# Performance work log

Hardware: AMD Instinct MI355X
Metric: run time of the kernel (lower is better)

Reference implementation:

```python
import jax, jax.numpy as jnp
import numpy as np

B = 4
HIDDEN = 256
NH, NL, NP = 8, 4, 4
DH = HIDDEN // NH
IMG = 256
SHAPES = ((64, 64), (32, 32), (16, 16), (8, 8))
CHS = (128, 256, 512, 512)
T = 3
NLAYERS = 6
S = sum(h * w for h, w in SHAPES)


def conv2d(x, w, b, pad):
    y = jax.lax.conv_general_dilated(x, w, (1, 1), [(pad, pad), (pad, pad)],
                                     dimension_numbers=('NCHW', 'OIHW', 'NCHW'))
    return y + b[None, :, None, None]


def group_norm(x, g, beta, groups=32, eps=1e-5):
    b, c, h, w = x.shape
    xg = x.reshape(b, groups, c // groups, h, w)
    mu = xg.mean((2, 3, 4), keepdims=True)
    var = ((xg - mu) ** 2).mean((2, 3, 4), keepdims=True)
    xg = (xg - mu) * jax.lax.rsqrt(var + eps)
    return xg.reshape(b, c, h, w) * g[None, :, None, None] + beta[None, :, None, None]


def layer_norm(x, g, b, eps=1e-5):
    mu = x.mean(-1, keepdims=True)
    var = ((x - mu) ** 2).mean(-1, keepdims=True)
    return (x - mu) * jax.lax.rsqrt(var + eps) * g + b


def pos_embed_sine(h, w, num_feats=128, temp=10000.0):
    # PositionEmbeddingSine with normalize=True, mask all-False
    scale = 2.0 * np.pi
    eps = 1e-6
    y = jnp.arange(1, h + 1, dtype=jnp.float32) / (h + eps) * scale
    x = jnp.arange(1, w + 1, dtype=jnp.float32) / (w + eps) * scale
    yy = jnp.broadcast_to(y[:, None], (h, w))
    xx = jnp.broadcast_to(x[None, :], (h, w))
    dim_t = temp ** (2.0 * (jnp.arange(num_feats) // 2).astype(jnp.float32) / num_feats)
    px = xx[..., None] / dim_t
    py = yy[..., None] / dim_t
    px = jnp.stack([jnp.sin(px[..., 0::2]), jnp.cos(px[..., 1::2])], -1).reshape(h, w, num_feats)
    py = jnp.stack([jnp.sin(py[..., 0::2]), jnp.cos(py[..., 1::2])], -1).reshape(h, w, num_feats)
    return jnp.concatenate([py, px], -1)  # (h, w, 2*num_feats)


def ms_deform(value, locs, attw):
    # value: (B,S,NH,DH); locs: (B,S,NH,NL,NP,2) normalized xy; attw: (B,S,NH,NL,NP)
    out = jnp.zeros((B, S, NH, DH), value.dtype)
    start = 0
    for l, (h, w) in enumerate(SHAPES):
        v = value[:, start:start + h * w]  # (B,hw,NH,DH)
        start += h * w
        gx = locs[:, :, :, l, :, 0] * w - 0.5  # grid_sample align_corners=False
        gy = locs[:, :, :, l, :, 1] * h - 0.5  # (B,S,NH,NP)
        x0 = jnp.floor(gx)
        y0 = jnp.floor(gy)
        wx1 = gx - x0
        wy1 = gy - y0
        acc = jnp.zeros((B, S, NH, NP, DH), value.dtype)
        for dy in (0, 1):
            for dx in (0, 1):
                xi = x0 + dx
                yi = y0 + dy
                wgt = (wx1 if dx else 1.0 - wx1) * (wy1 if dy else 1.0 - wy1)
                valid = ((xi >= 0) & (xi < w) & (yi >= 0) & (yi < h)).astype(value.dtype)
                xi_c = jnp.clip(xi, 0, w - 1).astype(jnp.int32)
                yi_c = jnp.clip(yi, 0, h - 1).astype(jnp.int32)
                idx = yi_c * w + xi_c  # (B,S,NH,NP)
                idx2 = idx.transpose(0, 1, 3, 2).reshape(B, S * NP, NH, 1)
                samp = jnp.take_along_axis(v, idx2, axis=1)  # (B,S*NP,NH,DH)
                samp = samp.reshape(B, S, NP, NH, DH).transpose(0, 1, 3, 2, 4)
                acc = acc + samp * (wgt * valid)[..., None]
        out = out + (acc * attw[:, :, :, l, :, None]).sum(3)
    return out.reshape(B, S, NH * DH)


def _forward(feat_t0_l0, feat_t0_l1, feat_t0_l2, feat_t0_l3,
             feat_t1_l0, feat_t1_l1, feat_t1_l2, feat_t1_l3,
             feat_t2_l0, feat_t2_l1, feat_t2_l2, feat_t2_l3,
             tfw,
             proj_w0, proj_b0, gn_g0, gn_b0,
             proj_w1, proj_b1, gn_g1, gn_b1,
             proj_w2, proj_b2, gn_g2, gn_b2,
             proj_w3, proj_b3, gn_g3, gn_b3,
             level_embed,
             off_w, off_b, aw_w, aw_b, val_w, val_b, out_w, out_b,
             ln1_g, ln1_b, ff1_w, ff1_b, ff2_w, ff2_b, ln2_g, ln2_b,
             c1_w, c1_b, c2_w, c2_b):
    feats = [[feat_t0_l0, feat_t0_l1, feat_t0_l2, feat_t0_l3],
             [feat_t1_l0, feat_t1_l1, feat_t1_l2, feat_t1_l3],
             [feat_t2_l0, feat_t2_l1, feat_t2_l2, feat_t2_l3]]
    proj = [(proj_w0, proj_b0, gn_g0, gn_b0), (proj_w1, proj_b1, gn_g1, gn_b1),
            (proj_w2, proj_b2, gn_g2, gn_b2), (proj_w3, proj_b3, gn_g3, gn_b3)]
    priors = (0, CHS[0], CHS[1], CHS[2])  # replicates original (buggy) prior indexing
    srcs, poss = [], []
    for l in range(NL):
        atf = jnp.stack([feats[t][l] for t in range(T)], 1)  # (B,T,C,H,W)
        wsl = jax.nn.softmax(tfw[:, priors[l]:priors[l] + CHS[l]], axis=0)  # (T,C)
        fused = (atf * wsl[None, :, :, None, None]).sum(1)
        pw, pb, gg, gb = proj[l]
        x = group_norm(conv2d(fused, pw, pb, 0), gg, gb)  # 1x1 proj + GN
        h, w = SHAPES[l]
        srcs.append(x.reshape(B, HIDDEN, h * w).transpose(0, 2, 1))
        pe = pos_embed_sine(h, w).reshape(h * w, HIDDEN) + level_embed[l]
        poss.append(jnp.broadcast_to(pe[None], (B, h * w, HIDDEN)))
    src = jnp.concatenate(srcs, 1)  # (B,S,256)
    pos = jnp.concatenate(poss, 1)
    # reference points (valid_ratios == 1 since masks are all False)
    refs = []
    for (h, w) in SHAPES:
        gy, gx = jnp.meshgrid((jnp.arange(h) + 0.5) / h, (jnp.arange(w) + 0.5) / w, indexing='ij')
        refs.append(jnp.stack([gx.ravel(), gy.ravel()], -1))
    ref = jnp.broadcast_to(jnp.concatenate(refs, 0)[None, :, None, :], (B, S, NL, 2)).astype(jnp.float32)
    norm_wh = jnp.array([[w, h] for (h, w) in SHAPES], jnp.float32)  # (NL,2) xy
    for i in range(NLAYERS):
        q = src + pos
        off = (q @ off_w[i].T + off_b[i]).reshape(B, S, NH, NL, NP, 2)
        aw = jax.nn.softmax((q @ aw_w[i].T + aw_b[i]).reshape(B, S, NH, NL * NP), -1).reshape(B, S, NH, NL, NP)
        val = (src @ val_w[i].T + val_b[i]).reshape(B, S, NH, DH)
        locs = ref[:, :, None, :, None, :] + off / norm_wh[None, None, None, :, None, :]
        attn = ms_deform(val, locs, aw) @ out_w[i].T + out_b[i]
        src = layer_norm(src + attn, ln1_g[i], ln1_b[i])
        ff = (jax.nn.relu(src @ ff1_w[i].T + ff1_b[i])) @ ff2_w[i].T + ff2_b[i]
        src = layer_norm(src + ff, ln2_g[i], ln2_b[i])
    h0, w0 = SHAPES[0]
    layer0 = src[:, :h0 * w0, :].reshape(B, h0, w0, HIDDEN).transpose(0, 3, 1, 2)
    pred = conv2d(jax.nn.relu(conv2d(layer0, c1_w, c1_b, 1)), c2_w, c2_b, 1)
    return jax.image.resize(pred, (B, pred.shape[1], IMG, IMG), method='bilinear')


def setup_inputs():
    key = jax.random.key(0)
    ks = iter(jax.random.split(key, 128))
    d = {}
    for t in range(T):
        for l, ((h, w), c) in enumerate(zip(SHAPES, CHS)):
            d['feat_t%d_l%d' % (t, l)] = jax.random.normal(next(ks), (B, c, h, w), jnp.float32)
    d['tfw'] = jax.random.normal(next(ks), (T, sum(CHS)), jnp.float32)
    for l, c in enumerate(CHS):
        d['proj_w%d' % l] = jax.random.normal(next(ks), (HIDDEN, c, 1, 1), jnp.float32) * 0.02
        d['proj_b%d' % l] = jnp.zeros((HIDDEN,), jnp.float32)
        d['gn_g%d' % l] = jnp.ones((HIDDEN,), jnp.float32)
        d['gn_b%d' % l] = jnp.zeros((HIDDEN,), jnp.float32)
    d['level_embed'] = jax.random.normal(next(ks), (NL, HIDDEN), jnp.float32)
    Lc = NLAYERS

    def w(shape, s=0.02):
        return jax.random.normal(next(ks), shape, jnp.float32) * s
    d['off_w'] = w((Lc, NH * NL * NP * 2, HIDDEN))
    d['off_b'] = w((Lc, NH * NL * NP * 2), 0.1)
    d['aw_w'] = w((Lc, NH * NL * NP, HIDDEN))
    d['aw_b'] = w((Lc, NH * NL * NP), 0.1)
    d['val_w'] = w((Lc, HIDDEN, HIDDEN))
    d['val_b'] = jnp.zeros((Lc, HIDDEN), jnp.float32)
    d['out_w'] = w((Lc, HIDDEN, HIDDEN))
    d['out_b'] = jnp.zeros((Lc, HIDDEN), jnp.float32)
    d['ln1_g'] = jnp.ones((Lc, HIDDEN), jnp.float32)
    d['ln1_b'] = jnp.zeros((Lc, HIDDEN), jnp.float32)
    d['ff1_w'] = w((Lc, 1024, HIDDEN))
    d['ff1_b'] = jnp.zeros((Lc, 1024), jnp.float32)
    d['ff2_w'] = w((Lc, HIDDEN, 1024))
    d['ff2_b'] = jnp.zeros((Lc, HIDDEN), jnp.float32)
    d['ln2_g'] = jnp.ones((Lc, HIDDEN), jnp.float32)
    d['ln2_b'] = jnp.zeros((Lc, HIDDEN), jnp.float32)
    d['c1_w'] = w((64, HIDDEN, 3, 3))
    d['c1_b'] = jnp.zeros((64,), jnp.float32)
    d['c2_w'] = w((2, 64, 3, 3))
    d['c2_b'] = jnp.zeros((2,), jnp.float32)
    return d


def reference(feat_t0_l0, feat_t0_l1, feat_t0_l2, feat_t0_l3,
              feat_t1_l0, feat_t1_l1, feat_t1_l2, feat_t1_l3,
              feat_t2_l0, feat_t2_l1, feat_t2_l2, feat_t2_l3,
              tfw,
              proj_w0, proj_b0, gn_g0, gn_b0,
              proj_w1, proj_b1, gn_g1, gn_b1,
              proj_w2, proj_b2, gn_g2, gn_b2,
              proj_w3, proj_b3, gn_g3, gn_b3,
              level_embed,
              off_w, off_b, aw_w, aw_b, val_w, val_b, out_w, out_b,
              ln1_g, ln1_b, ff1_w, ff1_b, ff2_w, ff2_b, ln2_g, ln2_b,
              c1_w, c1_b, c2_w, c2_b):
    return _forward(feat_t0_l0, feat_t0_l1, feat_t0_l2, feat_t0_l3,
                    feat_t1_l0, feat_t1_l1, feat_t1_l2, feat_t1_l3,
                    feat_t2_l0, feat_t2_l1, feat_t2_l2, feat_t2_l3,
                    tfw,
                    proj_w0, proj_b0, gn_g0, gn_b0,
                    proj_w1, proj_b1, gn_g1, gn_b1,
                    proj_w2, proj_b2, gn_g2, gn_b2,
                    proj_w3, proj_b3, gn_g3, gn_b3,
                    level_embed,
                    off_w, off_b, aw_w, aw_b, val_w, val_b, out_w, out_b,
                    ln1_g, ln1_b, ff1_w, ff1_b, ff2_w, ff2_b, ln2_g, ln2_b,
                    c1_w, c1_b, c2_w, c2_b)
```

## Files before the change

### kernel.cpp

```cpp
#include <hip/hip_runtime.h>
#include <math.h>

constexpr int kB = 4;
constexpr int kS = 5440;
constexpr int kH = 256;
constexpr int kNH = 8, kNL = 4, kNP = 4, kDH = 32;
constexpr int kM = kB * kS;
constexpr int kCHSUM = 1408;

typedef __attribute__((ext_vector_type(8))) short short8v;
typedef __attribute__((ext_vector_type(4))) short short4v;
typedef __attribute__((ext_vector_type(4))) float f32x4;
typedef __attribute__((ext_vector_type(2))) float fx2;
typedef __attribute__((ext_vector_type(16))) float f32x16;

__device__ inline short bf16rne(float f) {
    unsigned u = __float_as_uint(f);
    u += 0x7FFF + ((u >> 16) & 1);
    return (short)(u >> 16);
}
__device__ inline float bf2f(short s) {
    return __uint_as_float(((unsigned)(unsigned short)s) << 16);
}
__device__ inline int xcd_swz(int orig, int nwg) {
    int q = nwg >> 3, r = nwg & 7;
    int x = orig & 7, o = orig >> 3;
    return (x < r ? x*(q+1) : r*(q+1) + (x-r)*q) + o;
}
#define LSWZ(row, chunk) ((row)*40 + ((chunk) ^ ((row) & 24)))

__device__ inline void cv4(const float* __restrict__ in, short* __restrict__ out, int q)
{
    int i = q * 4;
    f32x4 v = *(const f32x4*)(in + i);
    short4v o;
    o[0]=bf16rne(v[0]); o[1]=bf16rne(v[1]); o[2]=bf16rne(v[2]); o[3]=bf16rne(v[3]);
    *(short4v*)(out + i) = o;
}
__global__ __launch_bounds__(256) void prep_all_kernel(
        const float* __restrict__ off_w, const float* __restrict__ aw_w,
        const float* __restrict__ off_b, const float* __restrict__ aw_b,
        const float* __restrict__ val_w, const float* __restrict__ out_w,
        const float* __restrict__ ff1w, const float* __restrict__ ff2w,
        const float* __restrict__ pw0, const float* __restrict__ pw1,
        const float* __restrict__ pw2, const float* __restrict__ pw3,
        const float* __restrict__ c1w, const float* __restrict__ c2w,
        short* __restrict__ Wcat, float* __restrict__ bcat,
        short* __restrict__ valwb, short* __restrict__ outwb,
        short* __restrict__ ff1wb, short* __restrict__ ff2wb,
        short* __restrict__ pwb, short* __restrict__ c1wb, float* __restrict__ c2wr)
{
    int idx = blockIdx.x * 256 + threadIdx.x;
    if (idx < 589824) {
        int col = idx & 255;
        int row = (idx >> 8) % 384;
        int i   = idx / (384*256);
        float v = (row < 256) ? off_w[((size_t)i*256 + row)*256 + col]
                              : aw_w[((size_t)i*128 + row-256)*256 + col];
        Wcat[idx] = bf16rne(v);
        return;
    }
    idx -= 589824;
    if (idx < 2304) {
        int row = idx % 384, i = idx / 384;
        bcat[idx] = (row < 256) ? off_b[i*256 + row] : aw_b[i*128 + row-256];
        return;
    }
    idx -= 2304;
    if (idx < 98304) { cv4(val_w, valwb, idx); return; }
    idx -= 98304;
    if (idx < 98304) { cv4(out_w, outwb, idx); return; }
    idx -= 98304;
    if (idx < 393216) { cv4(ff1w, ff1wb, idx); return; }
    idx -= 393216;
    if (idx < 393216) { cv4(ff2w, ff2wb, idx); return; }
    idx -= 393216;
    if (idx < 8192)  { cv4(pw0, pwb + 0,      idx); return; }
    idx -= 8192;
    if (idx < 16384) { cv4(pw1, pwb + 32768,  idx); return; }
    idx -= 16384;
    if (idx < 32768) { cv4(pw2, pwb + 98304,  idx); return; }
    idx -= 32768;
    if (idx < 32768) { cv4(pw3, pwb + 229376, idx); return; }
    idx -= 32768;
    if (idx < 147456) {
        int k = idx % 2304, o = idx / 2304;
        int kblk = k >> 8, c = k & 255;
        c1wb[idx] = bf16rne(c1w[(size_t)o*2304 + c*9 + kblk]);
        return;
    }
    idx -= 147456;
    if (idx < 1152) {
        int c = idx & 63, r = idx >> 6;
        int o = r / 9, kblk = r % 9;
        c2wr[idx] = c2w[((size_t)o*64 + c)*9 + kblk];
    }
}
constexpr int kPrepThreads = 589824+2304+98304+98304+393216+393216+8192+16384+32768+32768+147456+1152;


__global__ __launch_bounds__(256) void fuseT_kernel(const float* __restrict__ f0,
        const float* __restrict__ f1, const float* __restrict__ f2,
        const float* __restrict__ tfw, short* __restrict__ out,
        int c, int hw, int prior)
{
    __shared__ float tile[32][33];
    int p0 = blockIdx.x * 32;
    int c0 = blockIdx.y * 32;
    int b  = blockIdx.z;
    int tx  = threadIdx.x & 31;
    int ty8 = threadIdx.x >> 5;
    #pragma unroll
    for (int i = 0; i < 4; ++i) {
        int ch = c0 + ty8 + i*8;
        float t0 = tfw[0*kCHSUM + prior + ch];
        float t1 = tfw[1*kCHSUM + prior + ch];
        float t2 = tfw[2*kCHSUM + prior + ch];
        float m = fmaxf(t0, fmaxf(t1, t2));
        float e0 = expf(t0-m), e1 = expf(t1-m), e2 = expf(t2-m);
        float inv = 1.0f / (e0+e1+e2);
        size_t base = ((size_t)b*c + ch)*hw + p0 + tx;
        tile[ty8+i*8][tx] = f0[base]*(e0*inv) + f1[base]*(e1*inv) + f2[base]*(e2*inv);
    }
    __syncthreads();
    #pragma unroll
    for (int i = 0; i < 4; ++i) {
        int p = p0 + ty8 + i*8;
        out[((size_t)b*hw + p)*c + c0 + tx] = bf16rne(tile[tx][ty8+i*8]);
    }
}

__global__ __launch_bounds__(256) void gn_sum_kernel(const float* __restrict__ xbufT,
        float* __restrict__ gnstat, int nchunks)
{
    int chunk = blockIdx.x, b = blockIdx.y;
    int t = threadIdx.x;
    size_t base = ((size_t)b*nchunks + chunk) * 4096;
    float s = 0.f, q = 0.f;
    #pragma unroll
    for (int i = 0; i < 4; ++i) {
        f32x4 v = *(const f32x4*)(xbufT + base + i*1024 + t*4);
        s += v[0]+v[1]+v[2]+v[3];
        q += v[0]*v[0]+v[1]*v[1]+v[2]*v[2]+v[3]*v[3];
    }
    __shared__ float ls[256], lq[256];
    ls[t] = s; lq[t] = q; __syncthreads();
    if (t < 64) { ls[t] += ls[t+64]+ls[t+128]+ls[t+192];
                  lq[t] += lq[t+64]+lq[t+128]+lq[t+192]; }
    __syncthreads();
    if (t < 32) {
        float ss = ls[2*t] + ls[2*t+1];
        float qq = lq[2*t] + lq[2*t+1];
        size_t o = (((size_t)b*nchunks + chunk)*32 + t)*2;
        gnstat[o] = ss; gnstat[o+1] = qq;
    }
}

__global__ __launch_bounds__(256) void gn_fin_kernel(const float* __restrict__ gnstat,
        const float* __restrict__ gg, const float* __restrict__ gb,
        float* __restrict__ gnA, float* __restrict__ gnB, int nchunks, int hw)
{
    int b = blockIdx.x, t = threadIdx.x;
    int g = t >> 3, sub = t & 7;
    float s = 0.f, q = 0.f;
    for (int c = sub; c < nchunks; c += 8) {
        size_t o = (((size_t)b*nchunks + c)*32 + g)*2;
        s += gnstat[o]; q += gnstat[o+1];
    }
    __shared__ float ls[256], lq[256], gmu[32], ginv[32];
    ls[t] = s; lq[t] = q; __syncthreads();
    if (sub < 4) { ls[t] += ls[t+4]; lq[t] += lq[t+4]; } __syncthreads();
    if (sub < 2) { ls[t] += ls[t+2]; lq[t] += lq[t+2]; } __syncthreads();
    if (sub == 0) {
        float ss = ls[t] + ls[t+1], qq = lq[t] + lq[t+1];
        float n = 8.0f * hw;
        float mu = ss / n;
        float var = qq / n - mu*mu;
        gmu[g] = mu; ginv[g] = rsqrtf(var + 1e-5f);
    }
    __syncthreads();
    int ch = t;
    float A = ginv[ch>>3] * gg[ch];
    float B = gb[ch] - gmu[ch>>3] * A;
    gnA[b*256 + ch] = A;
    gnB[b*256 + ch] = B;
}

__global__ __launch_bounds__(256) void gn_apply_kernel(const float* __restrict__ xbufT,
        const float* __restrict__ gnA, const float* __restrict__ gnB,
        const float* __restrict__ pos, float* __restrict__ src,
        short* __restrict__ srcbf, short* __restrict__ qbf, int hw, int sbase)
{
    int E = hw * 256;
    size_t fl = (size_t)blockIdx.x*1024 + threadIdx.x*4;
    int b = (int)(fl / E);
    int off = (int)(fl - (size_t)b*E);
    int p = off >> 8, col = off & 255;
    f32x4 v = *(const f32x4*)(xbufT + fl);
    f32x4 A = *(const f32x4*)(gnA + b*256 + col);
    f32x4 Bv = *(const f32x4*)(gnB + b*256 + col);
    size_t si = ((size_t)b*kS + sbase + p)*256 + col;
    f32x4 pv = *(const f32x4*)(pos + si);
    f32x4 o;
    o[0]=v[0]*A[0]+Bv[0]; o[1]=v[1]*A[1]+Bv[1];
    o[2]=v[2]*A[2]+Bv[2]; o[3]=v[3]*A[3]+Bv[3];
    *(f32x4*)(src + si) = o;
    short4v sb, qb;
    sb[0]=bf16rne(o[0]); sb[1]=bf16rne(o[1]); sb[2]=bf16rne(o[2]); sb[3]=bf16rne(o[3]);
    qb[0]=bf16rne(o[0]+pv[0]); qb[1]=bf16rne(o[1]+pv[1]);
    qb[2]=bf16rne(o[2]+pv[2]); qb[3]=bf16rne(o[3]+pv[3]);
    *(short4v*)(srcbf + si) = sb;
    *(short4v*)(qbf + si) = qb;
}

__global__ __launch_bounds__(256) void pos_all_kernel(const float* __restrict__ lev,
                                                      float* __restrict__ pos)
{
    int idx = blockIdx.x * 256 + threadIdx.x;
    if (idx >= kS * 256) return;
    int ch = idx & 255;
    int p  = idx >> 8;
    int lvl, py, px, dim;
    if (p < 4096)      { lvl = 0; dim = 64; int l = p;        py = l >> 6; px = l & 63; }
    else if (p < 5120) { lvl = 1; dim = 32; int l = p - 4096; py = l >> 5; px = l & 31; }
    else if (p < 5376) { lvl = 2; dim = 16; int l = p - 5120; py = l >> 4; px = l & 15; }
    else               { lvl = 3; dim = 8;  int l = p - 5376; py = l >> 3; px = l & 7; }
    int c2 = ch & 127;
    int i  = c2 >> 1;
    float invdt = exp2f((float)i * -0.20762050593046015f);
    float t;
    if (ch < 128) t = (py + 1) / ((float)dim + 1e-6f) * 6.2831853071795864f;
    else          t = (px + 1) / ((float)dim + 1e-6f) * 6.2831853071795864f;
    float arg = t * invdt;
    float val = (c2 & 1) ? cosf(arg) : sinf(arg);
    val += lev[lvl*kH + ch];
    #pragma unroll
    for (int b = 0; b < kB; ++b)
        pos[(size_t)b*kS*256 + idx] = val;
}

template<int BM, int OUTMODE>
__global__ __launch_bounds__(256) void gemm32(const short* __restrict__ A,
        const short* __restrict__ W, const float* __restrict__ bias,
        float* __restrict__ C, short* __restrict__ Cb, int N, int K, int relu, int ncols)
{
    constexpr int FI = BM / 64;
    constexpr int NAV = (BM == 128) ? 4 : 2;
    __shared__ short Asm[2][BM * 40];
    __shared__ short Bsm[2][128 * 40];
    const int lin = xcd_swz(blockIdx.x, gridDim.x);
    const int bn  = (lin % ncols) * 128;
    const int bm  = (lin / ncols) * BM;
    const int t    = threadIdx.x;
    const int lane = t & 63;
    const int wid  = t >> 6;
    const int wr   = wid >> 1;
    const int wc   = wid & 1;
    const int l31  = lane & 31;
    const int hi8  = (lane >> 5) * 8;

    f32x16 acc[FI][2];
    #pragma unroll
    for (int i = 0; i < FI; ++i)
        #pragma unroll
        for (int j = 0; j < 2; ++j)
            acc[i][j] = (f32x16){0,0,0,0,0,0,0,0,0,0,0,0,0,0,0,0};

    int sa_r, sa_k;
    if constexpr (BM == 128) { sa_r = t >> 1; sa_k = (t & 1) * 32; }
    else                     { sa_r = t >> 2; sa_k = (t & 3) * 16; }
    const short* Aptr = A + (size_t)(bm + sa_r)*K + sa_k;
    const int sb_r = t >> 1;
    const int sb_k = (t & 1) * 32;
    const short* Wptr = W + (size_t)(bn + sb_r)*K + sb_k;

    short8v a[NAV], b[4];
    #pragma unroll
    for (int v = 0; v < NAV; ++v) a[v] = *(const short8v*)(Aptr + v*8);
    #pragma unroll
    for (int v = 0; v < 4; ++v)   b[v] = *(const short8v*)(Wptr + v*8);

    for (int k0 = 0; k0 < K; k0 += 64) {
        __syncthreads();
        if constexpr (BM == 128) {
            #pragma unroll
            for (int v = 0; v < 4; ++v) *(short8v*)&Asm[t & 1][LSWZ(sa_r, v*8)] = a[v];
        } else {
            #pragma unroll
            for (int v = 0; v < 2; ++v)
                *(short8v*)&Asm[sa_k >> 5][LSWZ(sa_r, (sa_k & 16) + v*8)] = a[v];
        }
        #pragma unroll
        for (int v = 0; v < 4; ++v) *(short8v*)&Bsm[t & 1][LSWZ(sb_r, v*8)] = b[v];
        __syncthreads();
        if (k0 + 64 < K) {
            #pragma unroll
            for (int v = 0; v < NAV; ++v) a[v] = *(const short8v*)(Aptr + k0 + 64 + v*8);
            #pragma unroll
            for (int v = 0; v < 4; ++v)   b[v] = *(const short8v*)(Wptr + k0 + 64 + v*8);
        }
        #pragma unroll
        for (int p = 0; p < 2; ++p)
            #pragma unroll
            for (int ks = 0; ks < 2; ++ks) {
                short8v af[FI], bfv[2];
                #pragma unroll
                for (int i = 0; i < FI; ++i)
                    af[i] = *(const short8v*)&Asm[p][LSWZ(wr*(BM/2) + i*32 + l31, ks*16 + hi8)];
                #pragma unroll
                for (int j = 0; j < 2; ++j)
                    bfv[j] = *(const short8v*)&Bsm[p][LSWZ(wc*64 + j*32 + l31, ks*16 + hi8)];
                #pragma unroll
                for (int i = 0; i < FI; ++i)
                    #pragma unroll
                    for (int j = 0; j < 2; ++j)
                        acc[i][j] = __builtin_amdgcn_mfma_f32_32x32x16_bf16(af[i], bfv[j], acc[i][j], 0, 0, 0);
            }
    }

    const int rbase = 4 * (lane >> 5);
    #pragma unroll
    for (int j = 0; j < 2; ++j) {
        int col = bn + wc*64 + j*32 + l31;
        float bz = bias[col];
        #pragma unroll
        for (int i = 0; i < FI; ++i) {
            int row0 = bm + wr*(BM/2) + i*32 + rbase;
            #pragma unroll
            for (int r = 0; r < 16; ++r) {
                int row = row0 + (r & 3) + 8*(r >> 2);
                float v = acc[i][j][r] + bz;
                if (relu) v = fmaxf(v, 0.f);
                if constexpr (OUTMODE == 0) C[(size_t)row*N + col] = v;
                else                        Cb[(size_t)row*N + col] = bf16rne(v);
            }
        }
    }
}

__global__ __launch_bounds__(256) void gemm_qv32(const short* __restrict__ Aq,
        const short* __restrict__ As, const short* __restrict__ W1,
        const short* __restrict__ W2, const float* __restrict__ b1,
        const float* __restrict__ b2, float* __restrict__ C1,
        short* __restrict__ Cb2)
{
    __shared__ short Asm[2][128 * 40];
    __shared__ short Bsm[2][128 * 40];
    const int lin = xcd_swz(blockIdx.x, gridDim.x);
    const int bn  = (lin % 5) * 128;
    const int bm  = (lin / 5) * 128;
    const bool qreg = bn < 384;
    const int K = 256;
    const int t    = threadIdx.x;
    const int lane = t & 63;
    const int wid  = t >> 6;
    const int wr   = wid >> 1;
    const int wc   = wid & 1;
    const int l31  = lane & 31;
    const int hi8  = (lane >> 5) * 8;
    const int sa_r = t >> 1;
    const int sa_p = t & 1;

    f32x16 acc[2][2];
    #pragma unroll
    for (int i = 0; i < 2; ++i)
        #pragma unroll
        for (int j = 0; j < 2; ++j)
            acc[i][j] = (f32x16){0,0,0,0,0,0,0,0,0,0,0,0,0,0,0,0};

    const short* Aptr = (qreg ? Aq : As) + (size_t)(bm + sa_r)*K + sa_p*32;
    const short* Wptr = (qreg ? (W1 + (size_t)(bn + sa_r)*K)
                              : (W2 + (size_t)(bn - 384 + sa_r)*K)) + sa_p*32;
    short8v a[4], b[4];
    #pragma unroll
    for (int v = 0; v < 4; ++v) { a[v] = *(const short8v*)(Aptr + v*8);
                                  b[v] = *(const short8v*)(Wptr + v*8); }

    for (int k0 = 0; k0 < K; k0 += 64) {
        __syncthreads();
        #pragma unroll
        for (int v = 0; v < 4; ++v) {
            *(short8v*)&Asm[sa_p][LSWZ(sa_r, v*8)] = a[v];
            *(short8v*)&Bsm[sa_p][LSWZ(sa_r, v*8)] = b[v];
        }
        __syncthreads();
        if (k0 + 64 < K) {
            #pragma unroll
            for (int v = 0; v < 4; ++v) {
                a[v] = *(const short8v*)(Aptr + k0 + 64 + v*8);
                b[v] = *(const short8v*)(Wptr + k0 + 64 + v*8);
            }
        }
        #pragma unroll
        for (int p = 0; p < 2; ++p)
            #pragma unroll
            for (int ks = 0; ks < 2; ++ks) {
                short8v af[2], bfv[2];
                #pragma unroll
                for (int i = 0; i < 2; ++i)
                    af[i] = *(const short8v*)&Asm[p][LSWZ(wr*64 + i*32 + l31, ks*16 + hi8)];
                #pragma unroll
                for (int j = 0; j < 2; ++j)
                    bfv[j] = *(const short8v*)&Bsm[p][LSWZ(wc*64 + j*32 + l31, ks*16 + hi8)];
                #pragma unroll
                for (int i = 0; i < 2; ++i)
                    #pragma unroll
                    for (int j = 0; j < 2; ++j)
                        acc[i][j] = __builtin_amdgcn_mfma_f32_32x32x16_bf16(af[i], bfv[j], acc[i][j], 0, 0, 0);
            }
    }

    const int rbase = 4 * (lane >> 5);
    if (bn == 256) {
        #pragma unroll
        for (int j = 0; j < 2; ++j) {
            int col = bn + wc*64 + j*32 + l31;
            float bz = b1[col];
            #pragma unroll
            for (int i = 0; i < 2; ++i) {
                int row0 = bm + wr*64 + i*32 + rbase;
                #pragma unroll
                for (int r = 0; r < 16; ++r) {
                    int row = row0 + (r & 3) + 8*(r >> 2);
                    float v = acc[i][j][r] + bz;
                    float m = v;
                    m = fmaxf(m, __shfl_xor(m, 1));
                    m = fmaxf(m, __shfl_xor(m, 2));
                    m = fmaxf(m, __shfl_xor(m, 4));
                    m = fmaxf(m, __shfl_xor(m, 8));
                    float e = expf(v - m);
                    float s = e;
                    s += __shfl_xor(s, 1);
                    s += __shfl_xor(s, 2);
                    s += __shfl_xor(s, 4);
                    s += __shfl_xor(s, 8);
                    C1[(size_t)row*384 + col] = e / s;
                }
            }
        }
    } else {
        #pragma unroll
        for (int j = 0; j < 2; ++j) {
            int col = bn + wc*64 + j*32 + l31;
            float bz = qreg ? b1[col] : b2[col - 384];
            #pragma unroll
            for (int i = 0; i < 2; ++i) {
                int row0 = bm + wr*64 + i*32 + rbase;
                #pragma unroll
                for (int r = 0; r < 16; ++r) {
                    int row = row0 + (r & 3) + 8*(r >> 2);
                    float v = acc[i][j][r] + bz;
                    if (qreg) C1[(size_t)row*384 + col] = v;
                    else      Cb2[(size_t)row*256 + col - 384] = bf16rne(v);
                }
            }
        }
    }
}

__global__ __launch_bounds__(256) void conv1_gemm_kernel(const short* __restrict__ srcbf,
        const short* __restrict__ Wr, const float* __restrict__ bias,
        float* __restrict__ C)
{
    __shared__ short Asm[2][128 * 40];
    __shared__ short Bsm[2][64 * 40];
    const int t    = threadIdx.x;
    const int bm   = blockIdx.x * 128;
    const int K    = 2304;
    const int lane = t & 63;
    const int wid  = t >> 6;
    const int wr   = wid >> 1;
    const int wc   = wid & 1;
    const int frow = lane & 15;
    const int g    = lane >> 4;
    const int sa_r = t >> 1;
    const int sa_p = t & 1;

    const int m  = bm + sa_r;
    const int bb = m >> 12, ys = (m >> 6) & 63, xs = m & 63;

    f32x4 acc[4][2];
    #pragma unroll
    for (int i = 0; i < 4; ++i)
        #pragma unroll
        for (int j = 0; j < 2; ++j)
            acc[i][j] = (f32x4){0.f,0.f,0.f,0.f};

    auto loadA = [&](int k0, short8v* r) {
        int kk = k0 + sa_p*32;
        int kblk = kk >> 8;
        int dyy = kblk / 3, dxx = kblk - dyy*3;
        int yy = ys + dyy - 1, xx = xs + dxx - 1;
        if (yy >= 0 && yy < 64 && xx >= 0 && xx < 64) {
            const short* p = srcbf + ((size_t)(bb*kS + yy*64 + xx))*256 + (kk & 255);
            #pragma unroll
            for (int v = 0; v < 4; ++v) r[v] = *(const short8v*)(p + v*8);
        } else {
            #pragma unroll
            for (int v = 0; v < 4; ++v) r[v] = (short8v){0,0,0,0,0,0,0,0};
        }
    };

    const int sb_r = t >> 2, sb_p = (t & 3) >> 1, sb_o = (t & 1) * 16;
    const short* Wptr = Wr + (size_t)sb_r*K + (t & 3)*16;
    short8v a[4], b[2];
    loadA(0, a);
    b[0] = *(const short8v*)Wptr;
    b[1] = *(const short8v*)(Wptr + 8);

    for (int k0 = 0; k0 < K; k0 += 64) {
        __syncthreads();
        #pragma unroll
        for (int v = 0; v < 4; ++v) *(short8v*)&Asm[sa_p][sa_r*40 + v*8] = a[v];
        *(short8v*)&Bsm[sb_p][sb_r*40 + sb_o]     = b[0];
        *(short8v*)&Bsm[sb_p][sb_r*40 + sb_o + 8] = b[1];
        __syncthreads();
        if (k0 + 64 < K) {
            loadA(k0 + 64, a);
            b[0] = *(const short8v*)(Wptr + k0 + 64);
            b[1] = *(const short8v*)(Wptr + k0 + 72);
        }
        #pragma unroll
        for (int p = 0; p < 2; ++p) {
            short8v af[4], bfv[2];
            #pragma unroll
            for (int i = 0; i < 4; ++i)
                af[i] = *(const short8v*)&Asm[p][(wr*64 + i*16 + frow)*40 + g*8];
            #pragma unroll
            for (int j = 0; j < 2; ++j)
                bfv[j] = *(const short8v*)&Bsm[p][(wc*32 + j*16 + frow)*40 + g*8];
            #pragma unroll
            for (int i = 0; i < 4; ++i)
                #pragma unroll
                for (int j = 0; j < 2; ++j)
                    acc[i][j] = __builtin_amdgcn_mfma_f32_16x16x32_bf16(af[i], bfv[j], acc[i][j], 0, 0, 0);
        }
    }

    #pragma unroll
    for (int j = 0; j < 2; ++j) {
        int col = wc*32 + j*16 + frow;
        float bz = bias[col];
        #pragma unroll
        for (int i = 0; i < 4; ++i) {
            int row = bm + wr*64 + i*16 + g*4;
            #pragma unroll
            for (int rr = 0; rr < 4; ++rr) {
                float v = fmaxf(acc[i][j][rr] + bz, 0.f);
                C[(size_t)(row + rr)*64 + col] = v;
            }
        }
    }
}

__global__ __launch_bounds__(256) void msdeform8_kernel(const short* __restrict__ val,
        const float* __restrict__ cat, short* __restrict__ msd)
{
    int blk  = xcd_swz(blockIdx.x, gridDim.x);
    int tid  = threadIdx.x;
    int d8   = tid & 3;
    int head = (tid >> 2) & 7;
    int bs   = blk*8 + (tid >> 5);
    int s  = bs % kS;
    int b  = bs / kS;
    float refx, refy;
    if (s < 4096)      { int loc = s;        refy = ((loc>>6)+0.5f)/64.f; refx = ((loc&63)+0.5f)/64.f; }
    else if (s < 5120) { int loc = s - 4096; refy = ((loc>>5)+0.5f)/32.f; refx = ((loc&31)+0.5f)/32.f; }
    else if (s < 5376) { int loc = s - 5120; refy = ((loc>>4)+0.5f)/16.f; refx = ((loc&15)+0.5f)/16.f; }
    else               { int loc = s - 5376; refy = ((loc>>3)+0.5f)/8.f;  refx = ((loc&7)+0.5f)/8.f; }
    const float* op = cat + (size_t)bs*384 + head*32;
    const float* ap = cat + (size_t)bs*384 + 256 + head*16;
    const short* vb = val + (size_t)b*kS*256 + head*32 + d8*8;
    const int WL[4] = {64,32,16,8};
    const int BASE[4] = {0,4096,5120,5376};
    fx2 acc0 = {0.f,0.f}, acc1 = {0.f,0.f}, acc2 = {0.f,0.f}, acc3 = {0.f,0.f};
    #pragma unroll
    for (int l = 0; l < 4; ++l) {
        int wl = WL[l], base = BASE[l];
        f32x4 o0 = *(const f32x4*)(op + l*8);
        f32x4 o1 = *(const f32x4*)(op + l*8 + 4);
        f32x4 av = *(const f32x4*)(ap + l*4);
        float oxs[4] = {o0[0], o0[2], o1[0], o1[2]};
        float oys[4] = {o0[1], o0[3], o1[1], o1[3]};
        #pragma unroll
        for (int p = 0; p < 4; ++p) {
            float gx = (refx + oxs[p]/wl)*wl - 0.5f;
            float gy = (refy + oys[p]/wl)*wl - 0.5f;
            float x0f = floorf(gx), y0f = floorf(gy);
            float wx1 = gx - x0f, wy1 = gy - y0f;
            int x0 = (int)x0f, y0 = (int)y0f;
            float a = av[p];
            #pragma unroll
            for (int dy = 0; dy < 2; ++dy) {
                int yi = y0 + dy;
                float wy = dy ? wy1 : 1.f - wy1;
                int vyok = (yi >= 0) & (yi < wl);
                int yc = min(max(yi, 0), wl - 1);
                #pragma unroll
                for (int dx = 0; dx < 2; ++dx) {
                    int xi = x0 + dx;
                    float wx = dx ? wx1 : 1.f - wx1;
                    int vok = vyok & (xi >= 0) & (xi < wl);
                    int xc = min(max(xi, 0), wl - 1);
                    float wgt = vok ? wx*wy*a : 0.f;
                    fx2 w2 = {wgt, wgt};
                    uint4 v = *(const uint4*)&vb[(size_t)(base + yc*wl + xc)*256];
                    fx2 t0, t1, t2, t3;
                    t0[0]=__uint_as_float(v.x << 16); t0[1]=__uint_as_float(v.x & 0xffff0000u);
                    t1[0]=__uint_as_float(v.y << 16); t1[1]=__uint_as_float(v.y & 0xffff0000u);
                    t2[0]=__uint_as_float(v.z << 16); t2[1]=__uint_as_float(v.z & 0xffff0000u);
                    t3[0]=__uint_as_float(v.w << 16); t3[1]=__uint_as_float(v.w & 0xffff0000u);
                    acc0 = t0 * w2 + acc0;
                    acc1 = t1 * w2 + acc1;
                    acc2 = t2 * w2 + acc2;
                    acc3 = t3 * w2 + acc3;
                }
            }
        }
    }
    short8v o;
    o[0]=bf16rne(acc0[0]); o[1]=bf16rne(acc0[1]);
    o[2]=bf16rne(acc1[0]); o[3]=bf16rne(acc1[1]);
    o[4]=bf16rne(acc2[0]); o[5]=bf16rne(acc2[1]);
    o[6]=bf16rne(acc3[0]); o[7]=bf16rne(acc3[1]);
    *(short8v*)&msd[(size_t)bs*256 + head*32 + d8*8] = o;
}

template<int WQ>
__global__ __launch_bounds__(256) void add_ln_kernel(float* __restrict__ src,
        const short* __restrict__ delta, const float* __restrict__ g,
        const float* __restrict__ bta, short* __restrict__ srcbf,
        short* __restrict__ qbf, const float* __restrict__ pos)
{
    int lane = threadIdx.x & 63;
    int row  = blockIdx.x*4 + (threadIdx.x >> 6);
    f32x4* s4 = (f32x4*)(src + (size_t)row*256);
    f32x4 x = s4[lane];
    short4v dd = *(const short4v*)&delta[(size_t)row*256 + lane*4];
    x[0]+=bf2f(dd[0]); x[1]+=bf2f(dd[1]); x[2]+=bf2f(dd[2]); x[3]+=bf2f(dd[3]);
    float s = x[0]+x[1]+x[2]+x[3];
    #pragma unroll
    for (int o = 1; o < 64; o <<= 1) s += __shfl_xor(s, o);
    float mu = s * (1.f/256.f);
    f32x4 xc;
    xc[0]=x[0]-mu; xc[1]=x[1]-mu; xc[2]=x[2]-mu; xc[3]=x[3]-mu;
    float s2 = xc[0]*xc[0]+xc[1]*xc[1]+xc[2]*xc[2]+xc[3]*xc[3];
    #pragma unroll
    for (int o = 1; o < 64; o <<= 1) s2 += __shfl_xor(s2, o);
    float inv = rsqrtf(s2*(1.f/256.f) + 1e-5f);
    const f32x4 gv = ((const f32x4*)g)[lane];
    const f32x4 bv = ((const f32x4*)bta)[lane];
    f32x4 o4;
    o4[0]=xc[0]*inv*gv[0]+bv[0]; o4[1]=xc[1]*inv*gv[1]+bv[1];
    o4[2]=xc[2]*inv*gv[2]+bv[2]; o4[3]=xc[3]*inv*gv[3]+bv[3];
    s4[lane] = o4;
    short4v sb;
    sb[0]=bf16rne(o4[0]); sb[1]=bf16rne(o4[1]); sb[2]=bf16rne(o4[2]); sb[3]=bf16rne(o4[3]);
    *(short4v*)&srcbf[(size_t)row*256 + lane*4] = sb;
    if constexpr (WQ) {
        f32x4 pv = ((const f32x4*)(pos + (size_t)row*256))[lane];
        short4v qb;
        qb[0]=bf16rne(o4[0]+pv[0]); qb[1]=bf16rne(o4[1]+pv[1]);
        qb[2]=bf16rne(o4[2]+pv[2]); qb[3]=bf16rne(o4[3]+pv[3]);
        *(short4v*)&qbf[(size_t)row*256 + lane*4] = qb;
    }
}

__global__ void conv2_kernel(const float* __restrict__ c1, const float* __restrict__ w,
                             const float* __restrict__ bias, float* __restrict__ pred)
{
    int idx = blockIdx.x * blockDim.x + threadIdx.x;
    int x = idx & 63;
    int y = (idx >> 6) & 63;
    int o = (idx >> 12) & 1;
    int b = idx >> 13;
    float acc = bias[o];
    #pragma unroll
    for (int dy = 0; dy < 3; ++dy) {
        int yy = y + dy - 1;
        if (yy < 0 || yy >= 64) continue;
        #pragma unroll
        for (int dx = 0; dx < 3; ++dx) {
            int xx = x + dx - 1;
            if (xx < 0 || xx >= 64) continue;
            const f32x4* sp = (const f32x4*)(c1 + ((size_t)(b*4096) + yy*64 + xx)*64);
            const f32x4* wp = (const f32x4*)(w + (o*9 + dy*3 + dx)*64);
            #pragma unroll
            for (int c = 0; c < 16; ++c) {
                f32x4 sv = sp[c], wv = wp[c];
                acc += sv[0]*wv[0] + sv[1]*wv[1] + sv[2]*wv[2] + sv[3]*wv[3];
            }
        }
    }
    pred[idx] = acc;
}

__global__ void resize_kernel(const float* __restrict__ pred, float* __restrict__ out)
{
    int idx = blockIdx.x * blockDim.x + threadIdx.x;
    int X = idx & 255;
    int Y = (idx >> 8) & 255;
    int c = (idx >> 16) & 1;
    int b = idx >> 17;
    float sx = (X + 0.5f)*0.25f - 0.5f;
    float sy = (Y + 0.5f)*0.25f - 0.5f;
    int x0 = (int)floorf(sx); float fx = sx - x0;
    int y0 = (int)floorf(sy); float fy = sy - y0;
    int x0c = min(max(x0, 0), 63), x1c = min(max(x0+1, 0), 63);
    int y0c = min(max(y0, 0), 63), y1c = min(max(y0+1, 0), 63);
    const float* p = pred + ((size_t)(b*2 + c))*4096;
    float v00 = p[y0c*64 + x0c], v01 = p[y0c*64 + x1c];
    float v10 = p[y1c*64 + x0c], v11 = p[y1c*64 + x1c];
    out[idx] = (1.f-fy)*((1.f-fx)*v00 + fx*v01) + fy*((1.f-fx)*v10 + fx*v11);
}

extern "C" void kernel_launch(void* const* d_in, const int* in_sizes, int n_in,
                              void* d_out, int out_size, void* d_ws, size_t ws_size,
                              hipStream_t stream)
{
    const float* F[3][4];
    for (int t = 0; t < 3; ++t)
        for (int l = 0; l < 4; ++l)
            F[t][l] = (const float*)d_in[t*4 + l];
    const float* tfw = (const float*)d_in[12];
    const float *pw[4], *pb[4], *gg[4], *gb[4];
    for (int l = 0; l < 4; ++l) {
        pw[l] = (const float*)d_in[13 + 4*l];
        pb[l] = (const float*)d_in[14 + 4*l];
        gg[l] = (const float*)d_in[15 + 4*l];
        gb[l] = (const float*)d_in[16 + 4*l];
    }
    const float* lev   = (const float*)d_in[29];
    const float* off_w = (const float*)d_in[30];
    const float* off_b = (const float*)d_in[31];
    const float* aw_w  = (const float*)d_in[32];
    const float* aw_b  = (const float*)d_in[33];
    const float* val_w = (const float*)d_in[34];
    const float* val_b = (const float*)d_in[35];
    const float* out_w = (const float*)d_in[36];
    const float* out_b = (const float*)d_in[37];
    const float* ln1g  = (const float*)d_in[38];
    const float* ln1b  = (const float*)d_in[39];
    const float* ff1w  = (const float*)d_in[40];
    const float* ff1b  = (const float*)d_in[41];
    const float* ff2w  = (const float*)d_in[42];
    const float* ff2b  = (const float*)d_in[43];
    const float* ln2g  = (const float*)d_in[44];
    const float* ln2b  = (const float*)d_in[45];
    const float* c1w   = (const float*)d_in[46];
    const float* c1b   = (const float*)d_in[47];
    const float* c2w   = (const float*)d_in[48];
    const float* c2b   = (const float*)d_in[49];

    const size_t N256 = (size_t)kB * kS * 256;
    float* ws    = (float*)d_ws;
    float* src   = ws;
    short* srcbf = (short*)(src + N256);
    short* qbf   = srcbf + N256;
    short* valbf = qbf + N256;
    short* msdbf = valbf + N256;
    short* warena= msdbf + N256;
    short* Wcat_bf = warena;
    short* valw_bf = Wcat_bf + 589824;
    short* outw_bf = valw_bf + 393216;
    short* ff1w_bf = outw_bf + 393216;
    short* ff2w_bf = ff1w_bf + 1572864;
    short* pw_bf   = ff2w_bf + 1572864;
    short* c1w_bf  = pw_bf + 360448;
    float* bcat  = (float*)(c1w_bf + 147456 + 128);
    float* gnstat= bcat + 4096;
    float* gnA   = gnstat + 65536;
    float* gnB   = gnA + 1024;
    float* c2wr  = gnB + 1024;
    float* pos   = c2wr + 1280;
    float* cat   = pos + N256;
    float* tmp   = cat + (size_t)kM*384;
    short* tmpbf = (short*)tmp;
    short* ffhbf = (short*)(tmp + N256);
    short* fusedT = (short*)cat;
    float* xbufT  = tmp;
    float* c1o   = (float*)valbf;
    float* pred  = (float*)msdbf;

    const int LVL_HWS[4]  = {4096, 1024, 256, 64};
    const int LVL_BASE[4] = {0, 4096, 5120, 5376};
    const int LVL_C[4]    = {128, 256, 512, 512};
    const int LVL_PRIOR[4]= {0, 128, 256, 512};
    const int PW_OFF[4]   = {0, 32768, 98304, 229376};

    prep_all_kernel<<<(kPrepThreads + 255)/256, 256, 0, stream>>>(
        off_w, aw_w, off_b, aw_b, val_w, out_w, ff1w, ff2w,
        pw[0], pw[1], pw[2], pw[3], c1w, c2w,
        Wcat_bf, bcat, valw_bf, outw_bf, ff1w_bf, ff2w_bf, pw_bf, c1w_bf, c2wr);

    pos_all_kernel<<<(kS*256 + 255)/256, 256, 0, stream>>>(lev, pos);
    for (int l = 0; l < 4; ++l) {
        int hw = LVL_HWS[l], c = LVL_C[l];
        dim3 gf(hw/32, c/32, kB);
        fuseT_kernel<<<gf, 256, 0, stream>>>(F[0][l], F[1][l], F[2][l], tfw,
                                             fusedT, c, hw, LVL_PRIOR[l]);
        int nwg = 2 * (kB*hw/64);
        gemm32<64,0><<<nwg, 256, 0, stream>>>(fusedT, pw_bf + PW_OFF[l], pb[l],
                                              xbufT, nullptr, 256, c, 0, 2);
        int nchunks = hw / 16;
        gn_sum_kernel<<<dim3(nchunks, kB), 256, 0, stream>>>(xbufT, gnstat, nchunks);
        gn_fin_kernel<<<kB, 256, 0, stream>>>(gnstat, gg[l], gb[l], gnA, gnB, nchunks, hw);
        gn_apply_kernel<<<(kB*hw*256)/1024, 256, 0, stream>>>(xbufT, gnA, gnB, pos,
                                                              src, srcbf, qbf, hw, LVL_BASE[l]);
    }

    for (int i = 0; i < 6; ++i) {
        gemm_qv32<<<5*(kM/128), 256, 0, stream>>>(qbf, srcbf,
                Wcat_bf + (size_t)i*384*256, valw_bf + (size_t)i*65536,
                bcat + i*384, val_b + i*256, cat, valbf);
        msdeform8_kernel<<<kM/8, 256, 0, stream>>>(valbf, cat, msdbf);
        gemm32<64,1><<<2*(kM/64), 256, 0, stream>>>(msdbf, outw_bf + (size_t)i*65536,
                                                    out_b + i*256, nullptr, tmpbf, 256, 256, 0, 2);
        add_ln_kernel<0><<<kM/4, 256, 0, stream>>>(src, tmpbf, ln1g + i*256, ln1b + i*256,
                                                   srcbf, nullptr, nullptr);
        gemm32<128,1><<<8*(kM/128), 256, 0, stream>>>(srcbf, ff1w_bf + (size_t)i*262144,
                                                      ff1b + i*1024, nullptr, ffhbf, 1024, 256, 1, 8);
        gemm32<64,1><<<2*(kM/64), 256, 0, stream>>>(ffhbf, ff2w_bf + (size_t)i*262144,
                                                    ff2b + i*256, nullptr, tmpbf, 256, 1024, 0, 2);
        add_ln_kernel<1><<<kM/4, 256, 0, stream>>>(src, tmpbf, ln2g + i*256, ln2b + i*256,
                                                   srcbf, qbf, pos);
    }

    {
        conv1_gemm_kernel<<<128, 256, 0, stream>>>(srcbf, c1w_bf, c1b, c1o);
        conv2_kernel<<<(kB*2*64*64)/256, 256, 0, stream>>>(c1o, c2wr, c2b, pred);
        resize_kernel<<<(kB*2*256*256)/256, 256, 0, stream>>>(pred, (float*)d_out);
    }
}
```

Before: 1.107 ms.

## Fuse output/FFN2 GEMMs with residual add and LayerNorm

Adds a gemm_ln kernel in which each block computes a full 64x256 output tile, adds bias and the residual, and does the LayerNorm reduction in registers and shared memory. It then writes src, srcbf and qbf directly, which removes the bf16 intermediate round trip and the separate add_ln launches. It also simplifies the sampling-coordinate math in msdeform and uses scalar fmas. In exchange, the grid has fewer blocks with wider N tiles, the accumulator is no longer rounded to bf16 before the residual add, and variance is computed as E[x^2]-mu^2.

Result: slower. 1.505 ms (+36.0%).

```diff
diff --git a/kernel.cpp b/kernel.cpp
--- a/kernel.cpp
+++ b/kernel.cpp
@@ -11,7 +11,6 @@
 typedef __attribute__((ext_vector_type(8))) short short8v;
 typedef __attribute__((ext_vector_type(4))) short short4v;
 typedef __attribute__((ext_vector_type(4))) float f32x4;
-typedef __attribute__((ext_vector_type(2))) float fx2;
 typedef __attribute__((ext_vector_type(16))) float f32x16;
 
 __device__ inline short bf16rne(float f) {
@@ -338,6 +337,129 @@
     }
 }
 
+template<int WQ>
+__global__ __launch_bounds__(256) void gemm_ln(const short* __restrict__ A,
+        const short* __restrict__ W, const float* __restrict__ bias,
+        const float* __restrict__ g, const float* __restrict__ bta,
+        float* __restrict__ src, short* __restrict__ srcbf,
+        short* __restrict__ qbf, const float* __restrict__ pos, int K)
+{
+    __shared__ short Asm[2][64 * 40];
+    __shared__ short Bsm[2][256 * 40];
+    __shared__ float lred[2][2][2][16][2];
+    const int t    = threadIdx.x;
+    const int bm   = blockIdx.x * 64;
+    const int lane = t & 63;
+    const int wid  = t >> 6;
+    const int wr   = wid >> 1;
+    const int wc   = wid & 1;
+    const int l31  = lane & 31;
+    const int hi   = lane >> 5;
+    const int hi8  = hi * 8;
+
+    f32x16 acc[4];
+    #pragma unroll
+    for (int j = 0; j < 4; ++j)
+        acc[j] = (f32x16){0,0,0,0,0,0,0,0,0,0,0,0,0,0,0,0};
+
+    const int sa_r = t >> 2;
+    const int sa_k = (t & 3) * 16;
+    const short* Aptr = A + (size_t)(bm + sa_r)*K + sa_k;
+    const short* Wptr = W + (size_t)t*K;
+
+    short8v a[2], b[8];
+    a[0] = *(const short8v*)(Aptr);
+    a[1] = *(const short8v*)(Aptr + 8);
+    #pragma unroll
+    for (int v = 0; v < 8; ++v) b[v] = *(const short8v*)(Wptr + v*8);
+
+    for (int k0 = 0; k0 < K; k0 += 64) {
+        __syncthreads();
+        *(short8v*)&Asm[sa_k >> 5][LSWZ(sa_r, (sa_k & 16) + 0)] = a[0];
+        *(short8v*)&Asm[sa_k >> 5][LSWZ(sa_r, (sa_k & 16) + 8)] = a[1];
+        #pragma unroll
+        for (int v = 0; v < 8; ++v)
+            *(short8v*)&Bsm[v >> 2][LSWZ(t, (v & 3)*8)] = b[v];
+        __syncthreads();
+        if (k0 + 64 < K) {
+            a[0] = *(const short8v*)(Aptr + k0 + 64);
+            a[1] = *(const short8v*)(Aptr + k0 + 72);
+            #pragma unroll
+            for (int v = 0; v < 8; ++v) b[v] = *(const short8v*)(Wptr + k0 + 64 + v*8);
+        }
+        #pragma unroll
+        for (int p = 0; p < 2; ++p)
+            #pragma unroll
+            for (int ks = 0; ks < 2; ++ks) {
+                short8v af = *(const short8v*)&Asm[p][LSWZ(wr*32 + l31, ks*16 + hi8)];
+                short8v bfv[4];
+                #pragma unroll
+                for (int j = 0; j < 4; ++j)
+                    bfv[j] = *(const short8v*)&Bsm[p][LSWZ(wc*128 + j*32 + l31, ks*16 + hi8)];
+                #pragma unroll
+                for (int j = 0; j < 4; ++j)
+                    acc[j] = __builtin_amdgcn_mfma_f32_32x32x16_bf16(af, bfv[j], acc[j], 0, 0, 0);
+            }
+    }
+
+    const int row0 = bm + wr*32 + 4*hi;
+    float rsum[16], rsq[16];
+    #pragma unroll
+    for (int r = 0; r < 16; ++r) { rsum[r] = 0.f; rsq[r] = 0.f; }
+    #pragma unroll
+    for (int j = 0; j < 4; ++j) {
+        int col = wc*128 + j*32 + l31;
+        float bz = bias[col];
+        #pragma unroll
+        for (int r = 0; r < 16; ++r) {
+            int row = row0 + (r & 3) + 8*(r >> 2);
+            float x = acc[j][r] + bz + src[(size_t)row*256 + col];
+            acc[j][r] = x;
+            rsum[r] += x;
+            rsq[r]  += x*x;
+        }
+    }
+    #pragma unroll
+    for (int o = 1; o < 32; o <<= 1) {
+        #pragma unroll
+        for (int r = 0; r < 16; ++r) {
+            rsum[r] += __shfl_xor(rsum[r], o);
+            rsq[r]  += __shfl_xor(rsq[r], o);
+        }
+    }
+    if (l31 == 0) {
+        #pragma unroll
+        for (int r = 0; r < 16; ++r) {
+            lred[wr][wc][hi][r][0] = rsum[r];
+            lred[wr][wc][hi][r][1] = rsq[r];
+        }
+    }
+    __syncthreads();
+    float mu[16], inv[16];
+    #pragma unroll
+    for (int r = 0; r < 16; ++r) {
+        float ts = rsum[r] + lred[wr][wc^1][hi][r][0];
+        float tq = rsq[r]  + lred[wr][wc^1][hi][r][1];
+        float m = ts * (1.f/256.f);
+        mu[r] = m;
+        inv[r] = rsqrtf(tq * (1.f/256.f) - m*m + 1e-5f);
+    }
+    #pragma unroll
+    for (int j = 0; j < 4; ++j) {
+        int col = wc*128 + j*32 + l31;
+        float gv = g[col], bv = bta[col];
+        #pragma unroll
+        for (int r = 0; r < 16; ++r) {
+            int row = row0 + (r & 3) + 8*(r >> 2);
+            size_t si = (size_t)row*256 + col;
+            float y = (acc[j][r] - mu[r]) * inv[r] * gv + bv;
+            src[si] = y;
+            srcbf[si] = bf16rne(y);
+            if constexpr (WQ) qbf[si] = bf16rne(y + pos[si]);
+        }
+    }
+}
+
 __global__ __launch_bounds__(256) void gemm_qv32(const short* __restrict__ Aq,
         const short* __restrict__ As, const short* __restrict__ W1,
         const short* __restrict__ W2, const float* __restrict__ b1,
@@ -573,10 +695,12 @@
     const short* vb = val + (size_t)b*kS*256 + head*32 + d8*8;
     const int WL[4] = {64,32,16,8};
     const int BASE[4] = {0,4096,5120,5376};
-    fx2 acc0 = {0.f,0.f}, acc1 = {0.f,0.f}, acc2 = {0.f,0.f}, acc3 = {0.f,0.f};
+    float acc[8] = {0.f,0.f,0.f,0.f,0.f,0.f,0.f,0.f};
     #pragma unroll
     for (int l = 0; l < 4; ++l) {
         int wl = WL[l], base = BASE[l];
+        float rxw = refx * wl - 0.5f;
+        float ryw = refy * wl - 0.5f;
         f32x4 o0 = *(const f32x4*)(op + l*8);
         f32x4 o1 = *(const f32x4*)(op + l*8 + 4);
         f32x4 av = *(const f32x4*)(ap + l*4);
@@ -584,8 +708,8 @@
         float oys[4] = {o0[1], o0[3], o1[1], o1[3]};
         #pragma unroll
         for (int p = 0; p < 4; ++p) {
-            float gx = (refx + oxs[p]/wl)*wl - 0.5f;
-            float gy = (refy + oys[p]/wl)*wl - 0.5f;
+            float gx = rxw + oxs[p];
+            float gy = ryw + oys[p];
             float x0f = floorf(gx), y0f = floorf(gy);
             float wx1 = gx - x0f, wy1 = gy - y0f;
             int x0 = (int)x0f, y0 = (int)y0f;
@@ -603,67 +727,23 @@
                     int vok = vyok & (xi >= 0) & (xi < wl);
                     int xc = min(max(xi, 0), wl - 1);
                     float wgt = vok ? wx*wy*a : 0.f;
-                    fx2 w2 = {wgt, wgt};
                     uint4 v = *(const uint4*)&vb[(size_t)(base + yc*wl + xc)*256];
-                    fx2 t0, t1, t2, t3;
-                    t0[0]=__uint_as_float(v.x << 16); t0[1]=__uint_as_float(v.x & 0xffff0000u);
-                    t1[0]=__uint_as_float(v.y << 16); t1[1]=__uint_as_float(v.y & 0xffff0000u);
-                    t2[0]=__uint_as_float(v.z << 16); t2[1]=__uint_as_float(v.z & 0xffff0000u);
-                    t3[0]=__uint_as_float(v.w << 16); t3[1]=__uint_as_float(v.w & 0xffff0000u);
-                    acc0 = t0 * w2 + acc0;
-                    acc1 = t1 * w2 + acc1;
-                    acc2 = t2 * w2 + acc2;
-                    acc3 = t3 * w2 + acc3;
+                    acc[0] = fmaf(__uint_as_float(v.x << 16),          wgt, acc[0]);
+                    acc[1] = fmaf(__uint_as_float(v.x & 0xffff0000u), wgt, acc[1]);
+                    acc[2] = fmaf(__uint_as_float(v.y << 16),          wgt, acc[2]);
+                    acc[3] = fmaf(__uint_as_float(v.y & 0xffff0000u), wgt, acc[3]);
+                    acc[4] = fmaf(__uint_as_float(v.z << 16),          wgt, acc[4]);
+                    acc[5] = fmaf(__uint_as_float(v.z & 0xffff0000u), wgt, acc[5]);
+                    acc[6] = fmaf(__uint_as_float(v.w << 16),          wgt, acc[6]);
+                    acc[7] = fmaf(__uint_as_float(v.w & 0xffff0000u), wgt, acc[7]);
                 }
             }
         }
     }
     short8v o;
-    o[0]=bf16rne(acc0[0]); o[1]=bf16rne(acc0[1]);
-    o[2]=bf16rne(acc1[0]); o[3]=bf16rne(acc1[1]);
-    o[4]=bf16rne(acc2[0]); o[5]=bf16rne(acc2[1]);
-    o[6]=bf16rne(acc3[0]); o[7]=bf16rne(acc3[1]);
+    #pragma unroll
+    for (int k = 0; k < 8; ++k) o[k] = bf16rne(acc[k]);
     *(short8v*)&msd[(size_t)bs*256 + head*32 + d8*8] = o;
-}
-
-template<int WQ>
-__global__ __launch_bounds__(256) void add_ln_kernel(float* __restrict__ src,
-        const short* __restrict__ delta, const float* __restrict__ g,
-        const float* __restrict__ bta, short* __restrict__ srcbf,
-        short* __restrict__ qbf, const float* __restrict__ pos)
-{
-    int lane = threadIdx.x & 63;
-    int row  = blockIdx.x*4 + (threadIdx.x >> 6);
-    f32x4* s4 = (f32x4*)(src + (size_t)row*256);
-    f32x4 x = s4[lane];
-    short4v dd = *(const short4v*)&delta[(size_t)row*256 + lane*4];
-    x[0]+=bf2f(dd[0]); x[1]+=bf2f(dd[1]); x[2]+=bf2f(dd[2]); x[3]+=bf2f(dd[3]);
-    float s = x[0]+x[1]+x[2]+x[3];
-    #pragma unroll
-    for (int o = 1; o < 64; o <<= 1) s += __shfl_xor(s, o);
-    float mu = s * (1.f/256.f);
-    f32x4 xc;
-    xc[0]=x[0]-mu; xc[1]=x[1]-mu; xc[2]=x[2]-mu; xc[3]=x[3]-mu;
-    float s2 = xc[0]*xc[0]+xc[1]*xc[1]+xc[2]*xc[2]+xc[3]*xc[3];
-    #pragma unroll
-    for (int o = 1; o < 64; o <<= 1) s2 += __shfl_xor(s2, o);
-    float inv = rsqrtf(s2*(1.f/256.f) + 1e-5f);
-    const f32x4 gv = ((const f32x4*)g)[lane];
-    const f32x4 bv = ((const f32x4*)bta)[lane];
-    f32x4 o4;
-    o4[0]=xc[0]*inv*gv[0]+bv[0]; o4[1]=xc[1]*inv*gv[1]+bv[1];
-    o4[2]=xc[2]*inv*gv[2]+bv[2]; o4[3]=xc[3]*inv*gv[3]+bv[3];
-    s4[lane] = o4;
-    short4v sb;
-    sb[0]=bf16rne(o4[0]); sb[1]=bf16rne(o4[1]); sb[2]=bf16rne(o4[2]); sb[3]=bf16rne(o4[3]);
-    *(short4v*)&srcbf[(size_t)row*256 + lane*4] = sb;
-    if constexpr (WQ) {
-        f32x4 pv = ((const f32x4*)(pos + (size_t)row*256))[lane];
-        short4v qb;
-        qb[0]=bf16rne(o4[0]+pv[0]); qb[1]=bf16rne(o4[1]+pv[1]);
-        qb[2]=bf16rne(o4[2]+pv[2]); qb[3]=bf16rne(o4[3]+pv[3]);
-        *(short4v*)&qbf[(size_t)row*256 + lane*4] = qb;
-    }
 }
 
 __global__ void conv2_kernel(const float* __restrict__ c1, const float* __restrict__ w,
@@ -775,7 +855,6 @@
     float* pos   = c2wr + 1280;
     float* cat   = pos + N256;
     float* tmp   = cat + (size_t)kM*384;
-    short* tmpbf = (short*)tmp;
     short* ffhbf = (short*)(tmp + N256);
     short* fusedT = (short*)cat;
     float* xbufT  = tmp;
@@ -814,16 +893,14 @@
                 Wcat_bf + (size_t)i*384*256, valw_bf + (size_t)i*65536,
                 bcat + i*384, val_b + i*256, cat, valbf);
         msdeform8_kernel<<<kM/8, 256, 0, stream>>>(valbf, cat, msdbf);
-        gemm32<64,1><<<2*(kM/64), 256, 0, stream>>>(msdbf, outw_bf + (size_t)i*65536,
-                                                    out_b + i*256, nullptr, tmpbf, 256, 256, 0, 2);
-        add_ln_kernel<0><<<kM/4, 256, 0, stream>>>(src, tmpbf, ln1g + i*256, ln1b + i*256,
-                                                   srcbf, nullptr, nullptr);
+        gemm_ln<0><<<kM/64, 256, 0, stream>>>(msdbf, outw_bf + (size_t)i*65536,
+                out_b + i*256, ln1g + i*256, ln1b + i*256,
+                src, srcbf, nullptr, nullptr, 256);
         gemm32<128,1><<<8*(kM/128), 256, 0, stream>>>(srcbf, ff1w_bf + (size_t)i*262144,
                                                       ff1b + i*1024, nullptr, ffhbf, 1024, 256, 1, 8);
-        gemm32<64,1><<<2*(kM/64), 256, 0, stream>>>(ffhbf, ff2w_bf + (size_t)i*262144,
-                                                    ff2b + i*256, nullptr, tmpbf, 256, 1024, 0, 2);
-        add_ln_kernel<1><<<kM/4, 256, 0, stream>>>(src, tmpbf, ln2g + i*256, ln2b + i*256,
-                                                   srcbf, qbf, pos);
+        gemm_ln<1><<<kM/64, 256, 0, stream>>>(ffhbf, ff2w_bf + (size_t)i*262144,
+                ff2b + i*256, ln2g + i*256, ln2b + i*256,
+                src, srcbf, qbf, pos, 1024);
     }
 
     {
```
